# Performance work log

Measured on AMD Instinct MI355X. Metric: run time of the kernel, lower is better.

The kernel has to match this reference:

```python
import jax, jax.numpy as jnp
import numpy as np

N_SRC = 100_000
N_NODES = 1_000_000
N_NEIGH = 20
RAW_DIM = 256
NEIGH_DIM = 128
MSG_DIM = 128


def setup_inputs() -> dict:
    key = jax.random.key(0)
    ks = jax.random.split(key, 8)
    s = 0.05
    return {
        "raw_messages": jax.random.normal(ks[0], (N_SRC, RAW_DIM), dtype=jnp.float32),
        "neighbors": jax.random.randint(ks[1], (N_SRC, N_NEIGH), 0, N_NODES, dtype=jnp.int64),
        "memory": jax.random.normal(ks[2], (N_NODES, NEIGH_DIM), dtype=jnp.float32),
        "W1": jax.random.normal(ks[3], (RAW_DIM, RAW_DIM // 2), dtype=jnp.float32) * s,
        "b1": jnp.zeros((RAW_DIM // 2,), dtype=jnp.float32),
        "W2": jax.random.normal(ks[4], (RAW_DIM // 2, MSG_DIM), dtype=jnp.float32) * s,
        "b2": jnp.zeros((MSG_DIM,), dtype=jnp.float32),
        "Wn": jax.random.normal(ks[5], (NEIGH_DIM, MSG_DIM), dtype=jnp.float32) * s,
        "bn": jnp.zeros((MSG_DIM,), dtype=jnp.float32),
    }


def reference(raw_messages, neighbors, memory, W1, b1, W2, b2, Wn, bn):
    # Gather neighbor memories: [N, K, D_neigh]
    neighbor_memories = memory[neighbors]
    # Mean-pool over the K sampled neighbors: [N, D_neigh]
    neighbor_agg = neighbor_memories.mean(axis=1)
    # message_sum MLP: Linear -> ReLU -> Linear -> ReLU
    h = jax.nn.relu(raw_messages @ W1 + b1)
    a = jax.nn.relu(h @ W2 + b2)
    # neighbor_sum MLP: Linear -> ReLU
    b = jax.nn.relu(neighbor_agg @ Wn + bn)
    return a + b
```

## Files before the change

kernel.cpp:

```cpp
#include <hip/hip_runtime.h>

#define N_SRC   100000
#define N_NEIGH 20
#define DRAW    256
#define DH      128
#define DMSG    128
#define DNEI    128
#define LDS_PAD 8

typedef __bf16 bf16x8 __attribute__((ext_vector_type(8)));
typedef float  floatx4 __attribute__((ext_vector_type(4)));

__global__ void convert_weights(const float* __restrict__ W1,
                                const float* __restrict__ W2,
                                const float* __restrict__ Wn,
                                __bf16* __restrict__ W1t,
                                __bf16* __restrict__ W2t,
                                __bf16* __restrict__ Wnt) {
    int i = blockIdx.x * 256 + threadIdx.x;
    if (i < 32768) {
        int n = i >> 8, k = i & 255;
        W1t[i] = (__bf16)W1[k * 128 + n];
    } else if (i < 49152) {
        int j = i - 32768;
        int n = j >> 7, k = j & 127;
        W2t[j] = (__bf16)W2[k * 128 + n];
    } else {
        int j = i - 49152;
        int n = j >> 7, k = j & 127;
        Wnt[j] = (__bf16)Wn[k * 128 + n];
    }
}

__global__ __launch_bounds__(256)
void gather_mean(const int*   __restrict__ neigh,
                 const float* __restrict__ memv,
                 float*       __restrict__ agg) {
    const int wid  = blockIdx.x * 4 + (threadIdx.x >> 6);
    const int lane = threadIdx.x & 63;
    if (wid >= N_SRC) return;

    int myidx = 0;
    if (lane < N_NEIGH) myidx = neigh[wid * N_NEIGH + lane];

    float2 v[N_NEIGH];
    #pragma unroll
    for (int n = 0; n < N_NEIGH; ++n) {
        int idx = __shfl(myidx, n, 64);
        v[n] = reinterpret_cast<const float2*>(memv + (size_t)idx * DNEI)[lane];
    }
    float sx = 0.f, sy = 0.f;
    #pragma unroll
    for (int n = 0; n < N_NEIGH; ++n) { sx += v[n].x; sy += v[n].y; }
    const float inv = 1.0f / N_NEIGH;
    float2 r; r.x = sx * inv; r.y = sy * inv;
    reinterpret_cast<float2*>(agg + (size_t)wid * DNEI)[lane] = r;
}

__global__ __launch_bounds__(256)
void mlp_kernel(const float* __restrict__ raw,
                const float* __restrict__ agg,
                const float* __restrict__ b1,
                const float* __restrict__ b2,
                const float* __restrict__ bn,
                const __bf16* __restrict__ W1t,
                const __bf16* __restrict__ W2t,
                const __bf16* __restrict__ Wnt,
                float* __restrict__ out) {
    __shared__ __bf16 hbuf[64][DH + LDS_PAD];

    const int tid  = threadIdx.x;
    const int s0   = blockIdx.x * 64;
    const int lane = tid & 63;
    const int wave = tid >> 6;
    const int mr   = lane & 15;
    const int quad = lane >> 4;

    const int rowg = s0 + wave * 16 + mr;
    const int rowc = rowg < N_SRC ? rowg : N_SRC - 1;

    float4 ag[8];
    {
        const float* ar3 = agg + (size_t)rowc * DNEI;
        #pragma unroll
        for (int i = 0; i < 4; ++i) {
            ag[2 * i]     = *reinterpret_cast<const float4*>(ar3 + i * 32 + quad * 8);
            ag[2 * i + 1] = *reinterpret_cast<const float4*>(ar3 + i * 32 + quad * 8 + 4);
        }
    }

    {
        const float* ar = raw + (size_t)rowc * DRAW;

        floatx4 acc[8];
        #pragma unroll
        for (int nt = 0; nt < 8; ++nt) { floatx4 z = {0.f,0.f,0.f,0.f}; acc[nt] = z; }

        #pragma unroll
        for (int kk = 0; kk < DRAW; kk += 32) {
            const int kb = kk + quad * 8;
            float4 a0 = *reinterpret_cast<const float4*>(ar + kb);
            float4 a1 = *reinterpret_cast<const float4*>(ar + kb + 4);
            bf16x8 af;
            af[0]=(__bf16)a0.x; af[1]=(__bf16)a0.y; af[2]=(__bf16)a0.z; af[3]=(__bf16)a0.w;
            af[4]=(__bf16)a1.x; af[5]=(__bf16)a1.y; af[6]=(__bf16)a1.z; af[7]=(__bf16)a1.w;
            #pragma unroll
            for (int nt = 0; nt < 8; ++nt) {
                bf16x8 bf = *reinterpret_cast<const bf16x8*>(
                    W1t + (nt * 16 + mr) * DRAW + kb);
                acc[nt] = __builtin_amdgcn_mfma_f32_16x16x32_bf16(af, bf, acc[nt], 0, 0, 0);
            }
        }
        #pragma unroll
        for (int nt = 0; nt < 8; ++nt) {
            const int col  = nt * 16 + mr;
            const float bias = b1[col];
            #pragma unroll
            for (int r = 0; r < 4; ++r) {
                int mrow = wave * 16 + quad * 4 + r;
                float v = acc[nt][r] + bias;
                hbuf[mrow][col] = (__bf16)(v > 0.f ? v : 0.f);
            }
        }
    }

    __syncthreads();

    {
        floatx4 acc2[8], acc3[8];
        #pragma unroll
        for (int nt = 0; nt < 8; ++nt) {
            floatx4 z = {0.f,0.f,0.f,0.f}; acc2[nt] = z; acc3[nt] = z;
        }

        #pragma unroll
        for (int kk = 0; kk < DH; kk += 32) {
            const int kb = kk + quad * 8;
            const int i  = kk >> 5;
            bf16x8 af2 = *reinterpret_cast<const bf16x8*>(&hbuf[wave * 16 + mr][kb]);
            bf16x8 af3;
            {
                float4 g0 = ag[2 * i], g1 = ag[2 * i + 1];
                af3[0]=(__bf16)g0.x; af3[1]=(__bf16)g0.y; af3[2]=(__bf16)g0.z; af3[3]=(__bf16)g0.w;
                af3[4]=(__bf16)g1.x; af3[5]=(__bf16)g1.y; af3[6]=(__bf16)g1.z; af3[7]=(__bf16)g1.w;
            }
            #pragma unroll
            for (int nt = 0; nt < 8; ++nt) {
                bf16x8 bw2 = *reinterpret_cast<const bf16x8*>(
                    W2t + (nt * 16 + mr) * DH + kb);
                acc2[nt] = __builtin_amdgcn_mfma_f32_16x16x32_bf16(af2, bw2, acc2[nt], 0, 0, 0);
                bf16x8 bw3 = *reinterpret_cast<const bf16x8*>(
                    Wnt + (nt * 16 + mr) * DNEI + kb);
                acc3[nt] = __builtin_amdgcn_mfma_f32_16x16x32_bf16(af3, bw3, acc3[nt], 0, 0, 0);
            }
        }

        #pragma unroll
        for (int nt = 0; nt < 8; ++nt) {
            const int col = nt * 16 + mr;
            const float bb2 = b2[col];
            const float bbn = bn[col];
            #pragma unroll
            for (int r = 0; r < 4; ++r) {
                int rowl = wave * 16 + quad * 4 + r;
                int rg   = s0 + rowl;
                if (rg < N_SRC) {
                    float va = acc2[nt][r] + bb2; va = va > 0.f ? va : 0.f;
                    float vb = acc3[nt][r] + bbn; vb = vb > 0.f ? vb : 0.f;
                    out[(size_t)rg * DMSG + col] = va + vb;
                }
            }
        }
    }
}

extern "C" void kernel_launch(void* const* d_in, const int* in_sizes, int n_in,
                              void* d_out, int out_size, void* d_ws, size_t ws_size,
                              hipStream_t stream) {
    const float* raw   = (const float*)d_in[0];
    const int*   neigh = (const int*)  d_in[1];
    const float* memv  = (const float*)d_in[2];
    const float* W1    = (const float*)d_in[3];
    const float* b1    = (const float*)d_in[4];
    const float* W2    = (const float*)d_in[5];
    const float* b2    = (const float*)d_in[6];
    const float* Wn    = (const float*)d_in[7];
    const float* bn    = (const float*)d_in[8];
    float* out = (float*)d_out;

    __bf16* W1t = (__bf16*)d_ws;
    __bf16* W2t = W1t + 32768;
    __bf16* Wnt = W2t + 16384;

    convert_weights<<<dim3(256), dim3(256), 0, stream>>>(W1, W2, Wn, W1t, W2t, Wnt);

    float* agg = out;
    gather_mean<<<dim3((N_SRC + 3) / 4), dim3(256), 0, stream>>>(neigh, memv, agg);

    const int nblocks = (N_SRC + 63) / 64;
    mlp_kernel<<<dim3(nblocks), dim3(256), 0, stream>>>(
        raw, agg, b1, b2, bn, W1t, W2t, Wnt, out);
}
```

Before: 900.6 us.

## Convert memory table to bf16 before gathering and split MLP into stages

Adds a path that converts the whole fp32 node-memory table to bf16 in workspace. That conversion runs in one kernel interleaved with the first GEMM, which writes the hidden activations as bf16. The neighbor gather then reads half-size bf16 rows and produces a bf16 mean, and a final kernel runs the two remaining GEMMs from the stored h and aggregate. This is meant to halve the bytes moved by the random gather. In exchange it adds a full streaming read and write of the memory table, plus an extra round trip through workspace for h. The new path only runs when the workspace is at least 320 MB; otherwise the old kernels run.

```diff
diff --git a/kernel.cpp b/kernel.cpp
--- a/kernel.cpp
+++ b/kernel.cpp
@@ -1,15 +1,31 @@
 #include <hip/hip_runtime.h>
 
-#define N_SRC   100000
-#define N_NEIGH 20
-#define DRAW    256
-#define DH      128
-#define DMSG    128
-#define DNEI    128
-#define LDS_PAD 8
+#define N_SRC    100000
+#define N_NODES  1000000
+#define N_NEIGH  20
+#define DRAW     256
+#define DH       128
+#define DMSG     128
+#define DNEI     128
+#define LDS_PAD  8
 
 typedef __bf16 bf16x8 __attribute__((ext_vector_type(8)));
 typedef float  floatx4 __attribute__((ext_vector_type(4)));
+typedef unsigned int uint32;
+
+#define OFF_W1T   (0ull)
+#define OFF_W2T   (64ull * 1024)
+#define OFF_WNT   (96ull * 1024)
+#define OFF_H     (1ull << 20)
+#define OFF_AGG   (32ull << 20)
+#define OFF_MEMBF (64ull << 20)
+#define WS_NEED   (320ull << 20)
+
+#define G1_BLOCKS   1563
+#define K2_PERIODS  521
+#define K2_TOTAL    (K2_PERIODS * 7)
+#define CV_BLOCKS   (K2_PERIODS * 4)
+#define NCHUNK      ((size_t)N_NODES * DNEI / 8)
 
 __global__ void convert_weights(const float* __restrict__ W1,
                                 const float* __restrict__ W2,
@@ -33,6 +49,192 @@
 }
 
 __global__ __launch_bounds__(256)
+void convert_and_gemm1(const float* __restrict__ raw,
+                       const float* __restrict__ memv,
+                       const float* __restrict__ b1,
+                       const __bf16* __restrict__ W1t,
+                       __bf16* __restrict__ membf,
+                       __bf16* __restrict__ h) {
+    __shared__ __bf16 hbuf[64][DH + LDS_PAD];
+
+    const int bid = blockIdx.x;
+    const int tid = threadIdx.x;
+    const int r   = bid % 7;
+    const int p   = bid / 7;
+
+    if (r >= 3) {
+        const int cvid = p * 4 + (r - 3);
+        size_t c = (size_t)cvid * 256 + tid;
+        const size_t stride = (size_t)CV_BLOCKS * 256;
+        for (; c < NCHUNK; c += stride) {
+            const floatx4* src = reinterpret_cast<const floatx4*>(memv + c * 8);
+            floatx4 a = __builtin_nontemporal_load(src);
+            floatx4 b = __builtin_nontemporal_load(src + 1);
+            bf16x8 o;
+            o[0]=(__bf16)a[0]; o[1]=(__bf16)a[1]; o[2]=(__bf16)a[2]; o[3]=(__bf16)a[3];
+            o[4]=(__bf16)b[0]; o[5]=(__bf16)b[1]; o[6]=(__bf16)b[2]; o[7]=(__bf16)b[3];
+            *reinterpret_cast<bf16x8*>(membf + c * 8) = o;
+        }
+        return;
+    }
+
+    const int g1id = p * 3 + r;
+    const int s0   = g1id * 64;
+    const int lane = tid & 63;
+    const int wave = tid >> 6;
+    const int mr   = lane & 15;
+    const int quad = lane >> 4;
+
+    {
+        int rowg = s0 + wave * 16 + mr;
+        int rowc = rowg < N_SRC ? rowg : N_SRC - 1;
+        const float* ar = raw + (size_t)rowc * DRAW;
+
+        floatx4 acc[8];
+        #pragma unroll
+        for (int nt = 0; nt < 8; ++nt) { floatx4 z = {0.f,0.f,0.f,0.f}; acc[nt] = z; }
+
+        #pragma unroll
+        for (int kk = 0; kk < DRAW; kk += 32) {
+            const int kb = kk + quad * 8;
+            floatx4 a0 = __builtin_nontemporal_load(
+                reinterpret_cast<const floatx4*>(ar + kb));
+            floatx4 a1 = __builtin_nontemporal_load(
+                reinterpret_cast<const floatx4*>(ar + kb) + 1);
+            bf16x8 af;
+            af[0]=(__bf16)a0[0]; af[1]=(__bf16)a0[1]; af[2]=(__bf16)a0[2]; af[3]=(__bf16)a0[3];
+            af[4]=(__bf16)a1[0]; af[5]=(__bf16)a1[1]; af[6]=(__bf16)a1[2]; af[7]=(__bf16)a1[3];
+            #pragma unroll
+            for (int nt = 0; nt < 8; ++nt) {
+                bf16x8 bf = *reinterpret_cast<const bf16x8*>(
+                    W1t + (nt * 16 + mr) * DRAW + kb);
+                acc[nt] = __builtin_amdgcn_mfma_f32_16x16x32_bf16(af, bf, acc[nt], 0, 0, 0);
+            }
+        }
+        #pragma unroll
+        for (int nt = 0; nt < 8; ++nt) {
+            const int col  = nt * 16 + mr;
+            const float bias = b1[col];
+            #pragma unroll
+            for (int rr = 0; rr < 4; ++rr) {
+                int mrow = wave * 16 + quad * 4 + rr;
+                float v = acc[nt][rr] + bias;
+                hbuf[mrow][col] = (__bf16)(v > 0.f ? v : 0.f);
+            }
+        }
+    }
+
+    __syncthreads();
+
+    const int cr = tid >> 4;
+    const int cc = (tid & 15) * 8;
+    #pragma unroll
+    for (int it = 0; it < 4; ++it) {
+        int row = cr + it * 16;
+        int rg  = s0 + row;
+        if (rg < N_SRC) {
+            *reinterpret_cast<bf16x8*>(h + (size_t)rg * DH + cc) =
+                *reinterpret_cast<const bf16x8*>(&hbuf[row][cc]);
+        }
+    }
+}
+
+__global__ __launch_bounds__(256)
+void gather_bf16(const int*    __restrict__ neigh,
+                 const __bf16* __restrict__ membf,
+                 __bf16*       __restrict__ aggb) {
+    int wid0 = blockIdx.x * 4 + (threadIdx.x >> 6);
+    const int wid  = __builtin_amdgcn_readfirstlane(wid0);
+    const int lane = threadIdx.x & 63;
+    if (wid >= N_SRC) return;
+
+    const int* nb = neigh + wid * N_NEIGH;
+    uint32 v[N_NEIGH];
+    #pragma unroll
+    for (int n = 0; n < N_NEIGH; ++n) {
+        int idx = nb[n];
+        v[n] = *reinterpret_cast<const uint32*>(
+            membf + (size_t)idx * DNEI + lane * 2);
+    }
+    float sx = 0.f, sy = 0.f;
+    #pragma unroll
+    for (int n = 0; n < N_NEIGH; ++n) {
+        sx += __builtin_bit_cast(float, v[n] << 16);
+        sy += __builtin_bit_cast(float, v[n] & 0xffff0000u);
+    }
+    const float inv = 1.0f / N_NEIGH;
+    __bf16 r0 = (__bf16)(sx * inv);
+    __bf16 r1 = (__bf16)(sy * inv);
+    union { __bf16 b[2]; uint32 u; } pk;
+    pk.b[0] = r0; pk.b[1] = r1;
+    *reinterpret_cast<uint32*>(aggb + (size_t)wid * DNEI + lane * 2) = pk.u;
+}
+
+__global__ __launch_bounds__(256)
+void gemm23(const __bf16* __restrict__ h,
+            const __bf16* __restrict__ aggb,
+            const float*  __restrict__ b2,
+            const float*  __restrict__ bn,
+            const __bf16* __restrict__ W2t,
+            const __bf16* __restrict__ Wnt,
+            float* __restrict__ out) {
+    const int tid  = threadIdx.x;
+    const int s0   = blockIdx.x * 64;
+    const int lane = tid & 63;
+    const int wave = tid >> 6;
+    const int mr   = lane & 15;
+    const int quad = lane >> 4;
+
+    const int rowg = s0 + wave * 16 + mr;
+    const int rowc = rowg < N_SRC ? rowg : N_SRC - 1;
+
+    bf16x8 af2[4], af3[4];
+    #pragma unroll
+    for (int i = 0; i < 4; ++i) {
+        const int kb = i * 32 + quad * 8;
+        af2[i] = *reinterpret_cast<const bf16x8*>(h    + (size_t)rowc * DH   + kb);
+        af3[i] = *reinterpret_cast<const bf16x8*>(aggb + (size_t)rowc * DNEI + kb);
+    }
+
+    floatx4 acc2[8], acc3[8];
+    #pragma unroll
+    for (int nt = 0; nt < 8; ++nt) {
+        floatx4 z = {0.f,0.f,0.f,0.f}; acc2[nt] = z; acc3[nt] = z;
+    }
+
+    #pragma unroll
+    for (int i = 0; i < 4; ++i) {
+        const int kb = i * 32 + quad * 8;
+        #pragma unroll
+        for (int nt = 0; nt < 8; ++nt) {
+            bf16x8 bw2 = *reinterpret_cast<const bf16x8*>(
+                W2t + (nt * 16 + mr) * DH + kb);
+            acc2[nt] = __builtin_amdgcn_mfma_f32_16x16x32_bf16(af2[i], bw2, acc2[nt], 0, 0, 0);
+            bf16x8 bw3 = *reinterpret_cast<const bf16x8*>(
+                Wnt + (nt * 16 + mr) * DNEI + kb);
+            acc3[nt] = __builtin_amdgcn_mfma_f32_16x16x32_bf16(af3[i], bw3, acc3[nt], 0, 0, 0);
+        }
+    }
+
+    #pragma unroll
+    for (int nt = 0; nt < 8; ++nt) {
+        const int col = nt * 16 + mr;
+        const float bb2 = b2[col];
+        const float bbn = bn[col];
+        #pragma unroll
+        for (int rr = 0; rr < 4; ++rr) {
+            int rowl = wave * 16 + quad * 4 + rr;
+            int rg   = s0 + rowl;
+            if (rg < N_SRC) {
+                float va = acc2[nt][rr] + bb2; va = va > 0.f ? va : 0.f;
+                float vb = acc3[nt][rr] + bbn; vb = vb > 0.f ? vb : 0.f;
+                out[(size_t)rg * DMSG + col] = va + vb;
+            }
+        }
+    }
+}
+
+__global__ __launch_bounds__(256)
 void gather_mean(const int*   __restrict__ neigh,
                  const float* __restrict__ memv,
                  float*       __restrict__ agg) {
@@ -53,8 +255,8 @@
     #pragma unroll
     for (int n = 0; n < N_NEIGH; ++n) { sx += v[n].x; sy += v[n].y; }
     const float inv = 1.0f / N_NEIGH;
-    float2 r; r.x = sx * inv; r.y = sy * inv;
-    reinterpret_cast<float2*>(agg + (size_t)wid * DNEI)[lane] = r;
+    float2 rr; rr.x = sx * inv; rr.y = sy * inv;
+    reinterpret_cast<float2*>(agg + (size_t)wid * DNEI)[lane] = rr;
 }
 
 __global__ __launch_bounds__(256)
@@ -91,7 +293,6 @@
 
     {
         const float* ar = raw + (size_t)rowc * DRAW;
-
         floatx4 acc[8];
         #pragma unroll
         for (int nt = 0; nt < 8; ++nt) { floatx4 z = {0.f,0.f,0.f,0.f}; acc[nt] = z; }
@@ -116,9 +317,9 @@
             const int col  = nt * 16 + mr;
             const float bias = b1[col];
             #pragma unroll
-            for (int r = 0; r < 4; ++r) {
-                int mrow = wave * 16 + quad * 4 + r;
-                float v = acc[nt][r] + bias;
+            for (int rr = 0; rr < 4; ++rr) {
+                int mrow = wave * 16 + quad * 4 + rr;
+                float v = acc[nt][rr] + bias;
                 hbuf[mrow][col] = (__bf16)(v > 0.f ? v : 0.f);
             }
         }
@@ -161,12 +362,12 @@
             const float bb2 = b2[col];
             const float bbn = bn[col];
             #pragma unroll
-            for (int r = 0; r < 4; ++r) {
-                int rowl = wave * 16 + quad * 4 + r;
+            for (int rr = 0; rr < 4; ++rr) {
+                int rowl = wave * 16 + quad * 4 + rr;
                 int rg   = s0 + rowl;
                 if (rg < N_SRC) {
-                    float va = acc2[nt][r] + bb2; va = va > 0.f ? va : 0.f;
-                    float vb = acc3[nt][r] + bbn; vb = vb > 0.f ? vb : 0.f;
+                    float va = acc2[nt][rr] + bb2; va = va > 0.f ? va : 0.f;
+                    float vb = acc3[nt][rr] + bbn; vb = vb > 0.f ? vb : 0.f;
                     out[(size_t)rg * DMSG + col] = va + vb;
                 }
             }
@@ -188,16 +389,27 @@
     const float* bn    = (const float*)d_in[8];
     float* out = (float*)d_out;
 
-    __bf16* W1t = (__bf16*)d_ws;
-    __bf16* W2t = W1t + 32768;
-    __bf16* Wnt = W2t + 16384;
+    __bf16* W1t = (__bf16*)((char*)d_ws + OFF_W1T);
+    __bf16* W2t = (__bf16*)((char*)d_ws + OFF_W2T);
+    __bf16* Wnt = (__bf16*)((char*)d_ws + OFF_WNT);
 
     convert_weights<<<dim3(256), dim3(256), 0, stream>>>(W1, W2, Wn, W1t, W2t, Wnt);
 
-    float* agg = out;
-    gather_mean<<<dim3((N_SRC + 3) / 4), dim3(256), 0, stream>>>(neigh, memv, agg);
-
-    const int nblocks = (N_SRC + 63) / 64;
-    mlp_kernel<<<dim3(nblocks), dim3(256), 0, stream>>>(
-        raw, agg, b1, b2, bn, W1t, W2t, Wnt, out);
-}
+    if (ws_size >= WS_NEED) {
+        __bf16* h     = (__bf16*)((char*)d_ws + OFF_H);
+        __bf16* aggb  = (__bf16*)((char*)d_ws + OFF_AGG);
+        __bf16* membf = (__bf16*)((char*)d_ws + OFF_MEMBF);
+
+        convert_and_gemm1<<<dim3(K2_TOTAL), dim3(256), 0, stream>>>(
+            raw, memv, b1, W1t, membf, h);
+        gather_bf16<<<dim3((N_SRC + 3) / 4), dim3(256), 0, stream>>>(
+            neigh, membf, aggb);
+        gemm23<<<dim3(G1_BLOCKS), dim3(256), 0, stream>>>(
+            h, aggb, b2, bn, W2t, Wnt, out);
+    } else {
+        float* agg = out;
+        gather_mean<<<dim3((N_SRC + 3) / 4), dim3(256), 0, stream>>>(neigh, memv, agg);
+        mlp_kernel<<<dim3(G1_BLOCKS), dim3(256), 0, stream>>>(
+            raw, agg, b1, b2, bn, W1t, W2t, Wnt, out);
+    }
+}
```

Measured after the change: 932.2 us. 3.5% more time.
